# Performance work log

Hardware: AMD Instinct MI355X
Metric: run time of the kernel (lower is better)

Reference implementation:

```python
import jax, jax.numpy as jnp
import numpy as np

N, E = 50000, 600000
IN, PE, H, L, K = 112, 16, 128, 64, 4


def setup_inputs() -> dict:
    key = jax.random.key(0)
    ks = jax.random.split(key, 8)
    x = jax.random.normal(ks[0], (N, IN), jnp.float32)
    edge_index = jax.random.randint(ks[1], (2, E), 0, N, dtype=jnp.int64)
    lap_pe = jax.random.normal(ks[2], (N, PE), jnp.float32)
    edge_weight = jax.random.uniform(ks[3], (E,), jnp.float32)
    s = lambda k, shp, fan: jax.random.normal(k, shp, jnp.float32) / np.sqrt(fan).astype(np.float32)
    W1 = s(ks[4], (K, IN + PE, H), IN + PE)
    b1 = jnp.zeros((H,), jnp.float32)
    W2 = s(ks[5], (K, H, H), H)
    b2 = jnp.zeros((H,), jnp.float32)
    Wmu = s(ks[6], (H, L), H)
    bmu = jnp.zeros((L,), jnp.float32)
    Wlv = s(ks[7], (H, L), H)
    blv = jnp.zeros((L,), jnp.float32)
    return dict(x=x, edge_index=edge_index, lap_pe=lap_pe, edge_weight=edge_weight,
                W1=W1, b1=b1, W2=W2, b2=b2, Wmu=Wmu, bmu=bmu, Wlv=Wlv, blv=blv)


def _cheb_conv(h, src, dst, w, W, b):
    """PyG ChebConv with precomputed scaled-Laplacian edge weights w.
    T_0 = h ; T_1 = That h ; T_k = 2 That T_{k-1} - T_{k-2}; out = sum_k T_k W_k + b."""
    n = h.shape[0]
    prop = lambda t: jax.ops.segment_sum(w[:, None] * t[src], dst, num_segments=n)
    Tx0 = h
    out = Tx0 @ W[0]
    Tx1 = prop(Tx0)
    out = out + Tx1 @ W[1]
    for k in range(2, W.shape[0]):
        Tx2 = 2.0 * prop(Tx1) - Tx0
        out = out + Tx2 @ W[k]
        Tx0, Tx1 = Tx1, Tx2
    return out + b


def reference(x, edge_index, lap_pe, edge_weight, W1, b1, W2, b2, Wmu, bmu, Wlv, blv):
    n = x.shape[0]
    src, dst = edge_index[0], edge_index[1]
    # sym-normalized Laplacian, lambda_max=2 -> That = L_sym - I = -D^-1/2 A D^-1/2
    deg = jax.ops.segment_sum(edge_weight, src, num_segments=n)
    dis = jnp.where(deg > 0, jax.lax.rsqrt(jnp.maximum(deg, 1e-12)), 0.0)
    w = -dis[src] * edge_weight * dis[dst]
    h = jnp.concatenate([x, lap_pe], axis=1)  # [N, in+pe]
    h = jax.nn.relu(_cheb_conv(h, src, dst, w, W1, b1))
    h = jax.nn.relu(_cheb_conv(h, src, dst, w, W2, b2))
    mu = h @ Wmu + bmu
    logvar = h @ Wlv + blv
    return (mu, logvar)
```

## Files before the change

kernel.cpp:

```cpp
#include <hip/hip_runtime.h>


typedef __bf16 bf16x8 __attribute__((ext_vector_type(8)));
typedef float f32x4 __attribute__((ext_vector_type(4)));
typedef unsigned int uint32;
typedef unsigned short ushort16;

__device__ inline ushort16 f2bf(float f) {
    uint32 x = __float_as_uint(f);
    uint32 r = x + 0x7fffu + ((x >> 16) & 1u);
    return (ushort16)(r >> 16);
}
__device__ inline float bflo(uint32 v) { return __uint_as_float(v << 16); }
__device__ inline float bfhi(uint32 v) { return __uint_as_float(v & 0xffff0000u); }


__global__ void k_deg_cnt(const int* __restrict__ src, const int* __restrict__ dst,
                          const float* __restrict__ ew, float* __restrict__ deg,
                          int* __restrict__ cnt, int E) {
    int e = blockIdx.x * blockDim.x + threadIdx.x;
    if (e >= E) return;
    atomicAdd(&deg[src[e]], ew[e]);
    atomicAdd(&cnt[dst[e]], 1);
}

__global__ void k_dis(const float* __restrict__ deg, float* __restrict__ dis, int N) {
    int i = blockIdx.x * blockDim.x + threadIdx.x;
    if (i >= N) return;
    float d = deg[i];
    dis[i] = d > 0.f ? rsqrtf(fmaxf(d, 1e-12f)) : 0.f;
}

__global__ void k_scan_blk(const int* __restrict__ cnt, int* __restrict__ row_ptr,
                           int* __restrict__ blk_sums, int N) {
    __shared__ int wsum[4];
    const int tid = threadIdx.x;
    const int base = blockIdx.x * 1024 + tid * 4;
    int4 v = make_int4(0, 0, 0, 0);
    if (base + 3 < N) v = *(const int4*)&cnt[base];
    else {
        if (base + 0 < N) v.x = cnt[base + 0];
        if (base + 1 < N) v.y = cnt[base + 1];
        if (base + 2 < N) v.z = cnt[base + 2];
    }
    const int tsum = v.x + v.y + v.z + v.w;
    const int lane = tid & 63;
    const int wv = tid >> 6;
    int incl = tsum;
    #pragma unroll
    for (int off = 1; off < 64; off <<= 1) {
        int t = __shfl_up(incl, off);
        if (lane >= off) incl += t;
    }
    if (lane == 63) wsum[wv] = incl;
    __syncthreads();
    int woff = 0;
    #pragma unroll
    for (int w = 0; w < 4; ++w) if (w < wv) woff += wsum[w];
    const int excl = woff + incl - tsum;
    if (base + 0 < N) row_ptr[base + 0] = excl;
    if (base + 1 < N) row_ptr[base + 1] = excl + v.x;
    if (base + 2 < N) row_ptr[base + 2] = excl + v.x + v.y;
    if (base + 3 < N) row_ptr[base + 3] = excl + v.x + v.y + v.z;
    if (tid == 255) blk_sums[blockIdx.x] = woff + incl;
}

__global__ void k_scan_top(int* __restrict__ blk_sums, int* __restrict__ row_ptr,
                           int nblk, int N) {
    const int lane = threadIdx.x;
    int v = (lane < nblk) ? blk_sums[lane] : 0;
    int incl = v;
    #pragma unroll
    for (int off = 1; off < 64; off <<= 1) {
        int t = __shfl_up(incl, off);
        if (lane >= off) incl += t;
    }
    if (lane < nblk) blk_sums[lane] = incl - v;
    if (lane == 63) row_ptr[N] = incl;
}

__global__ void k_scan_fix(int* __restrict__ row_ptr, int* __restrict__ cursor,
                           const int* __restrict__ blk_sums, int N) {
    int i = blockIdx.x * blockDim.x + threadIdx.x;
    if (i >= N) return;
    int v = row_ptr[i] + blk_sums[i >> 10];
    row_ptr[i] = v;
    cursor[i] = v;
}

__global__ void k_scatter(const int* __restrict__ src, const int* __restrict__ dst,
                          const float* __restrict__ ew, const float* __restrict__ dis,
                          int* __restrict__ cursor, int* __restrict__ csr_src,
                          float* __restrict__ csr_w, int E) {
    int e = blockIdx.x * blockDim.x + threadIdx.x;
    if (e >= E) return;
    int s = src[e], d = dst[e];
    float wv = -dis[s] * ew[e] * dis[d];
    int pos = atomicAdd(&cursor[d], 1);
    csr_src[pos] = s;
    csr_w[pos] = wv;
}


__global__ void k_concat_bf16(const float* __restrict__ x, const float* __restrict__ pe,
                              uint32* __restrict__ h, int N) {
    int i = blockIdx.x * blockDim.x + threadIdx.x;
    if (i >= N * 64) return;
    int node = i >> 6, p = i & 63;
    float f0, f1;
    if (p < 56) { f0 = x[node * 112 + p * 2]; f1 = x[node * 112 + p * 2 + 1]; }
    else { int q = (p - 56) * 2; f0 = pe[node * 16 + q]; f1 = pe[node * 16 + q + 1]; }
    h[i] = (uint32)f2bf(f0) | ((uint32)f2bf(f1) << 16);
}


__global__ void k_pack_w(const float* __restrict__ W, ushort16* __restrict__ Wp, int KS) {
    int t = blockIdx.x * blockDim.x + threadIdx.x;
    if (t >= KS * 8 * 64) return;
    int l = t & 63, c = (t >> 6) & 7, ks = t >> 9;
    int k0 = ks * 32 + (l >> 4) * 8;
    int col = c * 16 + (l & 15);
    uint4 o;
    uint32 v[8];
    #pragma unroll
    for (int j = 0; j < 8; ++j) v[j] = f2bf(W[(size_t)(k0 + j) * 128 + col]);
    o.x = v[0] | (v[1] << 16); o.y = v[2] | (v[3] << 16);
    o.z = v[4] | (v[5] << 16); o.w = v[6] | (v[7] << 16);
    *(uint4*)(Wp + (size_t)t * 8) = o;
}

__global__ void k_pack_head(const float* __restrict__ Wm, const float* __restrict__ Wl,
                            ushort16* __restrict__ Wp) {
    int t = blockIdx.x * blockDim.x + threadIdx.x;
    if (t >= 4 * 8 * 64) return;
    int l = t & 63, c = (t >> 6) & 7, ks = t >> 9;
    int k0 = ks * 32 + (l >> 4) * 8;
    int cc = c * 16 + (l & 15);
    const float* Ws = (cc < 64) ? Wm : Wl;
    int col = cc & 63;
    uint4 o;
    uint32 v[8];
    #pragma unroll
    for (int j = 0; j < 8; ++j) v[j] = f2bf(Ws[(size_t)(k0 + j) * 64 + col]);
    o.x = v[0] | (v[1] << 16); o.y = v[2] | (v[3] << 16);
    o.z = v[4] | (v[5] << 16); o.w = v[6] | (v[7] << 16);
    *(uint4*)(Wp + (size_t)t * 8) = o;
}


template<bool HAS_SUB>
__global__ void k_prop_bf16(const ushort16* __restrict__ tin, const ushort16* __restrict__ sub,
                            float scale, const int* __restrict__ row_ptr,
                            const int* __restrict__ csr_src, const float* __restrict__ csr_w,
                            uint32* __restrict__ out, int N) {
    int wid = (blockIdx.x * blockDim.x + threadIdx.x) >> 6;
    int lane = threadIdx.x & 63;
    if (wid >= N) return;
    int beg = row_ptr[wid], end = row_ptr[wid + 1];
    float ax = 0.f, ay = 0.f;
    for (int base = beg; base < end; base += 64) {
        int m = end - base; if (m > 64) m = 64;
        int si = 0; float wv = 0.f;
        if (lane < m) { si = csr_src[base + lane]; wv = csr_w[base + lane]; }
        int j = 0;
        for (; j + 3 < m; j += 4) {
            int s0 = __shfl(si, j),     s1 = __shfl(si, j + 1);
            int s2 = __shfl(si, j + 2), s3 = __shfl(si, j + 3);
            float w0 = __shfl(wv, j),     w1 = __shfl(wv, j + 1);
            float w2 = __shfl(wv, j + 2), w3 = __shfl(wv, j + 3);
            uint32 v0 = *(const uint32*)((const ushort16*)tin + (size_t)s0 * 128 + lane * 2);
            uint32 v1 = *(const uint32*)((const ushort16*)tin + (size_t)s1 * 128 + lane * 2);
            uint32 v2 = *(const uint32*)((const ushort16*)tin + (size_t)s2 * 128 + lane * 2);
            uint32 v3 = *(const uint32*)((const ushort16*)tin + (size_t)s3 * 128 + lane * 2);
            ax = fmaf(w0, bflo(v0), ax); ay = fmaf(w0, bfhi(v0), ay);
            ax = fmaf(w1, bflo(v1), ax); ay = fmaf(w1, bfhi(v1), ay);
            ax = fmaf(w2, bflo(v2), ax); ay = fmaf(w2, bfhi(v2), ay);
            ax = fmaf(w3, bflo(v3), ax); ay = fmaf(w3, bfhi(v3), ay);
        }
        for (; j < m; ++j) {
            int s0 = __shfl(si, j);
            float w0 = __shfl(wv, j);
            uint32 v0 = *(const uint32*)((const ushort16*)tin + (size_t)s0 * 128 + lane * 2);
            ax = fmaf(w0, bflo(v0), ax); ay = fmaf(w0, bfhi(v0), ay);
        }
    }
    float ox = scale * ax, oy = scale * ay;
    if (HAS_SUB) {
        uint32 sv = *(const uint32*)((const ushort16*)sub + (size_t)wid * 128 + lane * 2);
        ox -= bflo(sv); oy -= bfhi(sv);
    }
    out[(size_t)wid * 64 + lane] = (uint32)f2bf(ox) | ((uint32)f2bf(oy) << 16);
}


template<bool RELU>
__launch_bounds__(256)
__global__ void k_mfma_gemm512(const ushort16* __restrict__ t0, const ushort16* __restrict__ t1,
                               const ushort16* __restrict__ t2, const ushort16* __restrict__ t3,
                               const ushort16* __restrict__ Wp, const float* __restrict__ bias,
                               ushort16* __restrict__ C, int N) {
    const int lane = threadIdx.x & 63;
    const int wave = threadIdx.x >> 6;
    const int brow = blockIdx.x * 128 + wave * 32;
    int r0 = brow + (lane & 15);
    int r1 = r0 + 16;
    if (r0 >= N) r0 = N - 1;
    if (r1 >= N) r1 = N - 1;
    const int kg8 = (lane >> 4) * 8;
    f32x4 acc[2][8] = {};
    #pragma unroll
    for (int t = 0; t < 4; ++t) {
        const ushort16* __restrict__ A = (t == 0) ? t0 : (t == 1) ? t1 : (t == 2) ? t2 : t3;
        const ushort16* a0p = A + (size_t)r0 * 128 + kg8;
        const ushort16* a1p = A + (size_t)r1 * 128 + kg8;
        #pragma unroll
        for (int ks2 = 0; ks2 < 4; ++ks2) {
            bf16x8 a0 = *(const bf16x8*)(a0p + ks2 * 32);
            bf16x8 a1 = *(const bf16x8*)(a1p + ks2 * 32);
            const ushort16* bp = Wp + (size_t)((t * 4 + ks2) * 8 * 64 + lane) * 8;
            #pragma unroll
            for (int c = 0; c < 8; ++c) {
                bf16x8 b = *(const bf16x8*)(bp + c * 512);
                acc[0][c] = __builtin_amdgcn_mfma_f32_16x16x32_bf16(a0, b, acc[0][c], 0, 0, 0);
                acc[1][c] = __builtin_amdgcn_mfma_f32_16x16x32_bf16(a1, b, acc[1][c], 0, 0, 0);
            }
        }
    }
    const int col0 = lane & 15;
    const int rj = (lane >> 4) * 4;
    #pragma unroll
    for (int m = 0; m < 2; ++m) {
        #pragma unroll
        for (int c = 0; c < 8; ++c) {
            float bv = bias[c * 16 + col0];
            #pragma unroll
            for (int j = 0; j < 4; ++j) {
                int row = brow + m * 16 + rj + j;
                if (row < N) {
                    float v = acc[m][c][j] + bv;
                    if (RELU) v = fmaxf(v, 0.f);
                    C[(size_t)row * 128 + c * 16 + col0] = f2bf(v);
                }
            }
        }
    }
}


__launch_bounds__(256)
__global__ void k_mfma_head(const ushort16* __restrict__ A, const ushort16* __restrict__ Wp,
                            const float* __restrict__ bm, const float* __restrict__ bl,
                            float* __restrict__ out, int N) {
    const int lane = threadIdx.x & 63;
    const int wave = threadIdx.x >> 6;
    const int brow = blockIdx.x * 128 + wave * 32;
    int r0 = brow + (lane & 15);
    int r1 = r0 + 16;
    if (r0 >= N) r0 = N - 1;
    if (r1 >= N) r1 = N - 1;
    const int kg8 = (lane >> 4) * 8;
    f32x4 acc[2][8] = {};
    const ushort16* a0p = A + (size_t)r0 * 128 + kg8;
    const ushort16* a1p = A + (size_t)r1 * 128 + kg8;
    #pragma unroll
    for (int ks = 0; ks < 4; ++ks) {
        bf16x8 a0 = *(const bf16x8*)(a0p + ks * 32);
        bf16x8 a1 = *(const bf16x8*)(a1p + ks * 32);
        const ushort16* bp = Wp + (size_t)(ks * 8 * 64 + lane) * 8;
        #pragma unroll
        for (int c = 0; c < 8; ++c) {
            bf16x8 b = *(const bf16x8*)(bp + c * 512);
            acc[0][c] = __builtin_amdgcn_mfma_f32_16x16x32_bf16(a0, b, acc[0][c], 0, 0, 0);
            acc[1][c] = __builtin_amdgcn_mfma_f32_16x16x32_bf16(a1, b, acc[1][c], 0, 0, 0);
        }
    }
    const int col0 = lane & 15;
    const int rj = (lane >> 4) * 4;
    #pragma unroll
    for (int m = 0; m < 2; ++m) {
        #pragma unroll
        for (int c = 0; c < 8; ++c) {
            int gcol = (c & 3) * 16 + col0;
            float bv = (c < 4) ? bm[gcol] : bl[gcol];
            size_t hoff = (c < 4) ? 0 : (size_t)N * 64;
            #pragma unroll
            for (int j = 0; j < 4; ++j) {
                int row = brow + m * 16 + rj + j;
                if (row < N)
                    out[hoff + (size_t)row * 64 + gcol] = acc[m][c][j] + bv;
            }
        }
    }
}


extern "C" void kernel_launch(void* const* d_in, const int* in_sizes, int n_in,
                              void* d_out, int out_size, void* d_ws, size_t ws_size,
                              hipStream_t stream) {
    const float* x   = (const float*)d_in[0];
    const int*   ei  = (const int*)d_in[1];
    const float* pe  = (const float*)d_in[2];
    const float* ew  = (const float*)d_in[3];
    const float* W1  = (const float*)d_in[4];
    const float* b1  = (const float*)d_in[5];
    const float* W2  = (const float*)d_in[6];
    const float* b2  = (const float*)d_in[7];
    const float* Wmu = (const float*)d_in[8];
    const float* bmu = (const float*)d_in[9];
    const float* Wlv = (const float*)d_in[10];
    const float* blv = (const float*)d_in[11];

    const int N = in_sizes[0] / 112;
    const int E = in_sizes[1] / 2;
    const int* src = ei;
    const int* dst = ei + E;

    char* ws = (char*)d_ws;
    size_t off = 0;
    auto alloc = [&](size_t bytes) -> char* {
        char* p = ws + off;
        off = (off + bytes + 255) & ~(size_t)255;
        return p;
    };
    float* deg     = (float*)alloc((size_t)N * 4);
    int*   cnt     = (int*)  alloc((size_t)N * 4);
    float* dis     = (float*)alloc((size_t)N * 4);
    int*   row_ptr = (int*)  alloc((size_t)(N + 1) * 4);
    int*   cursor  = (int*)  alloc((size_t)N * 4);
    int*   blk_sums= (int*)  alloc((size_t)256 * 4);
    int*   csr_src = (int*)  alloc((size_t)E * 4);
    float* csr_w   = (float*)alloc((size_t)E * 4);
    ushort16* W1p  = (ushort16*)alloc((size_t)512 * 128 * 2);
    ushort16* W2p  = (ushort16*)alloc((size_t)512 * 128 * 2);
    ushort16* WHp  = (ushort16*)alloc((size_t)128 * 128 * 2);
    ushort16* B0 = (ushort16*)alloc((size_t)N * 128 * 2);
    ushort16* B1 = (ushort16*)alloc((size_t)N * 128 * 2);
    ushort16* B2 = (ushort16*)alloc((size_t)N * 128 * 2);
    ushort16* B3 = (ushort16*)alloc((size_t)N * 128 * 2);
    ushort16* B4 = (ushort16*)alloc((size_t)N * 128 * 2);

    hipMemsetAsync(deg, 0, (size_t)N * 4, stream);
    hipMemsetAsync(cnt, 0, (size_t)N * 4, stream);

    const int eb = (E + 255) / 256;
    const int nb = (N + 255) / 256;
    const int pb = (N + 3) / 4;
    const int gb = (N + 127) / 128;
    const int nblk = (N + 1023) / 1024;

    k_deg_cnt<<<eb, 256, 0, stream>>>(src, dst, ew, deg, cnt, E);
    k_dis<<<nb, 256, 0, stream>>>(deg, dis, N);
    k_scan_blk<<<nblk, 256, 0, stream>>>(cnt, row_ptr, blk_sums, N);
    k_scan_top<<<1, 64, 0, stream>>>(blk_sums, row_ptr, nblk, N);
    k_scan_fix<<<nb, 256, 0, stream>>>(row_ptr, cursor, blk_sums, N);
    k_scatter<<<eb, 256, 0, stream>>>(src, dst, ew, dis, cursor, csr_src, csr_w, E);
    k_concat_bf16<<<(N * 64 + 255) / 256, 256, 0, stream>>>(x, pe, (uint32*)B0, N);
    k_pack_w<<<(16 * 8 * 64 + 255) / 256, 256, 0, stream>>>(W1, W1p, 16);
    k_pack_w<<<(16 * 8 * 64 + 255) / 256, 256, 0, stream>>>(W2, W2p, 16);
    k_pack_head<<<(4 * 8 * 64 + 255) / 256, 256, 0, stream>>>(Wmu, Wlv, WHp);

    k_prop_bf16<false><<<pb, 256, 0, stream>>>(B0, nullptr, 1.f, row_ptr, csr_src, csr_w, (uint32*)B1, N);
    k_prop_bf16<true ><<<pb, 256, 0, stream>>>(B1, B0, 2.f, row_ptr, csr_src, csr_w, (uint32*)B2, N);
    k_prop_bf16<true ><<<pb, 256, 0, stream>>>(B2, B1, 2.f, row_ptr, csr_src, csr_w, (uint32*)B3, N);
    k_mfma_gemm512<true><<<gb, 256, 0, stream>>>(B0, B1, B2, B3, W1p, b1, B4, N);

    k_prop_bf16<false><<<pb, 256, 0, stream>>>(B4, nullptr, 1.f, row_ptr, csr_src, csr_w, (uint32*)B0, N);
    k_prop_bf16<true ><<<pb, 256, 0, stream>>>(B0, B4, 2.f, row_ptr, csr_src, csr_w, (uint32*)B1, N);
    k_prop_bf16<true ><<<pb, 256, 0, stream>>>(B1, B0, 2.f, row_ptr, csr_src, csr_w, (uint32*)B2, N);
    k_mfma_gemm512<true><<<gb, 256, 0, stream>>>(B4, B0, B1, B2, W2p, b2, B3, N);

    k_mfma_head<<<gb, 256, 0, stream>>>(B3, WHp, bmu, blv, (float*)d_out, N);
}
```

Baseline: 357.0 us.

## Fold Chebyshev recurrence into weights and use plain powers of the propagation operator

Rewrites the Chebyshev basis as plain powers of That (T2=2P²-I, T3=4P³-3P) and folds the recombination into pre-transformed weight matrices. The propagation kernels then drop the scale and subtract steps. The CSR build stores src and weight interleaved as int2 and takes each slot from the count atomic, removing the cursor scan and the second atomic pass. Weight-packing and dis kernels are merged to cut launches. Dropping the recurrence changes rounding, since the bf16 intermediate powers are combined in the GEMM instead of step by step.

```diff
diff --git a/kernel.cpp b/kernel.cpp
--- a/kernel.cpp
+++ b/kernel.cpp
@@ -17,18 +17,11 @@
 
 __global__ void k_deg_cnt(const int* __restrict__ src, const int* __restrict__ dst,
                           const float* __restrict__ ew, float* __restrict__ deg,
-                          int* __restrict__ cnt, int E) {
+                          int* __restrict__ cnt, int* __restrict__ pos, int E) {
     int e = blockIdx.x * blockDim.x + threadIdx.x;
     if (e >= E) return;
     atomicAdd(&deg[src[e]], ew[e]);
-    atomicAdd(&cnt[dst[e]], 1);
-}
-
-__global__ void k_dis(const float* __restrict__ deg, float* __restrict__ dis, int N) {
-    int i = blockIdx.x * blockDim.x + threadIdx.x;
-    if (i >= N) return;
-    float d = deg[i];
-    dis[i] = d > 0.f ? rsqrtf(fmaxf(d, 1e-12f)) : 0.f;
+    pos[e] = atomicAdd(&cnt[dst[e]], 1);
 }
 
 __global__ void k_scan_blk(const int* __restrict__ cnt, int* __restrict__ row_ptr,
@@ -79,26 +72,24 @@
     if (lane == 63) row_ptr[N] = incl;
 }
 
-__global__ void k_scan_fix(int* __restrict__ row_ptr, int* __restrict__ cursor,
-                           const int* __restrict__ blk_sums, int N) {
+__global__ void k_fix_dis(int* __restrict__ row_ptr, const int* __restrict__ blk_sums,
+                          const float* __restrict__ deg, float* __restrict__ dis, int N) {
     int i = blockIdx.x * blockDim.x + threadIdx.x;
     if (i >= N) return;
-    int v = row_ptr[i] + blk_sums[i >> 10];
-    row_ptr[i] = v;
-    cursor[i] = v;
+    row_ptr[i] += blk_sums[i >> 10];
+    float d = deg[i];
+    dis[i] = d > 0.f ? rsqrtf(fmaxf(d, 1e-12f)) : 0.f;
 }
 
 __global__ void k_scatter(const int* __restrict__ src, const int* __restrict__ dst,
                           const float* __restrict__ ew, const float* __restrict__ dis,
-                          int* __restrict__ cursor, int* __restrict__ csr_src,
-                          float* __restrict__ csr_w, int E) {
+                          const int* __restrict__ row_ptr, const int* __restrict__ pos,
+                          int2* __restrict__ csr, int E) {
     int e = blockIdx.x * blockDim.x + threadIdx.x;
     if (e >= E) return;
     int s = src[e], d = dst[e];
     float wv = -dis[s] * ew[e] * dis[d];
-    int pos = atomicAdd(&cursor[d], 1);
-    csr_src[pos] = s;
-    csr_w[pos] = wv;
+    csr[row_ptr[d] + pos[e]] = make_int2(s, __float_as_int(wv));
 }
 
 
@@ -114,45 +105,55 @@
 }
 
 
-__global__ void k_pack_w(const float* __restrict__ W, ushort16* __restrict__ Wp, int KS) {
+__device__ inline float wtrans(const float* __restrict__ W, int kb, size_t o) {
+    switch (kb) {
+        case 0:  return W[o] - W[o + 32768];
+        case 1:  return W[o + 16384] - 3.f * W[o + 49152];
+        case 2:  return 2.f * W[o + 32768];
+        default: return 4.f * W[o + 49152];
+    }
+}
+
+__global__ void k_pack_all(const float* __restrict__ W1, const float* __restrict__ W2,
+                           const float* __restrict__ Wm, const float* __restrict__ Wl,
+                           ushort16* __restrict__ W1p, ushort16* __restrict__ W2p,
+                           ushort16* __restrict__ WHp) {
     int t = blockIdx.x * blockDim.x + threadIdx.x;
-    if (t >= KS * 8 * 64) return;
-    int l = t & 63, c = (t >> 6) & 7, ks = t >> 9;
-    int k0 = ks * 32 + (l >> 4) * 8;
-    int col = c * 16 + (l & 15);
-    uint4 o;
     uint32 v[8];
-    #pragma unroll
-    for (int j = 0; j < 8; ++j) v[j] = f2bf(W[(size_t)(k0 + j) * 128 + col]);
-    o.x = v[0] | (v[1] << 16); o.y = v[2] | (v[3] << 16);
-    o.z = v[4] | (v[5] << 16); o.w = v[6] | (v[7] << 16);
-    *(uint4*)(Wp + (size_t)t * 8) = o;
-}
-
-__global__ void k_pack_head(const float* __restrict__ Wm, const float* __restrict__ Wl,
-                            ushort16* __restrict__ Wp) {
-    int t = blockIdx.x * blockDim.x + threadIdx.x;
-    if (t >= 4 * 8 * 64) return;
-    int l = t & 63, c = (t >> 6) & 7, ks = t >> 9;
-    int k0 = ks * 32 + (l >> 4) * 8;
-    int cc = c * 16 + (l & 15);
-    const float* Ws = (cc < 64) ? Wm : Wl;
-    int col = cc & 63;
-    uint4 o;
-    uint32 v[8];
-    #pragma unroll
-    for (int j = 0; j < 8; ++j) v[j] = f2bf(Ws[(size_t)(k0 + j) * 64 + col]);
-    o.x = v[0] | (v[1] << 16); o.y = v[2] | (v[3] << 16);
-    o.z = v[4] | (v[5] << 16); o.w = v[6] | (v[7] << 16);
-    *(uint4*)(Wp + (size_t)t * 8) = o;
-}
-
-
-template<bool HAS_SUB>
-__global__ void k_prop_bf16(const ushort16* __restrict__ tin, const ushort16* __restrict__ sub,
-                            float scale, const int* __restrict__ row_ptr,
-                            const int* __restrict__ csr_src, const float* __restrict__ csr_w,
-                            uint32* __restrict__ out, int N) {
+    if (t < 16384) {
+        const float* W = (t < 8192) ? W1 : W2;
+        ushort16* Wp = (t < 8192) ? W1p : W2p;
+        int tt = t & 8191;
+        int l = tt & 63, c = (tt >> 6) & 7, ks = tt >> 9;
+        int kb = ks >> 2;
+        int r0 = (ks & 3) * 32 + (l >> 4) * 8;
+        int col = c * 16 + (l & 15);
+        #pragma unroll
+        for (int j = 0; j < 8; ++j)
+            v[j] = f2bf(wtrans(W, kb, (size_t)(r0 + j) * 128 + col));
+        uint4 o;
+        o.x = v[0] | (v[1] << 16); o.y = v[2] | (v[3] << 16);
+        o.z = v[4] | (v[5] << 16); o.w = v[6] | (v[7] << 16);
+        *(uint4*)(Wp + (size_t)tt * 8) = o;
+    } else if (t < 16384 + 2048) {
+        int tt = t - 16384;
+        int l = tt & 63, c = (tt >> 6) & 7, ks = tt >> 9;
+        int k0 = ks * 32 + (l >> 4) * 8;
+        int cc = c * 16 + (l & 15);
+        const float* Ws = (cc < 64) ? Wm : Wl;
+        int col = cc & 63;
+        #pragma unroll
+        for (int j = 0; j < 8; ++j) v[j] = f2bf(Ws[(size_t)(k0 + j) * 64 + col]);
+        uint4 o;
+        o.x = v[0] | (v[1] << 16); o.y = v[2] | (v[3] << 16);
+        o.z = v[4] | (v[5] << 16); o.w = v[6] | (v[7] << 16);
+        *(uint4*)(WHp + (size_t)tt * 8) = o;
+    }
+}
+
+
+__global__ void k_prop(const uint32* __restrict__ tin, const int2* __restrict__ csr,
+                       const int* __restrict__ row_ptr, uint32* __restrict__ out, int N) {
     int wid = (blockIdx.x * blockDim.x + threadIdx.x) >> 6;
     int lane = threadIdx.x & 63;
     if (wid >= N) return;
@@ -160,36 +161,18 @@
     float ax = 0.f, ay = 0.f;
     for (int base = beg; base < end; base += 64) {
         int m = end - base; if (m > 64) m = 64;
-        int si = 0; float wv = 0.f;
-        if (lane < m) { si = csr_src[base + lane]; wv = csr_w[base + lane]; }
-        int j = 0;
-        for (; j + 3 < m; j += 4) {
-            int s0 = __shfl(si, j),     s1 = __shfl(si, j + 1);
-            int s2 = __shfl(si, j + 2), s3 = __shfl(si, j + 3);
-            float w0 = __shfl(wv, j),     w1 = __shfl(wv, j + 1);
-            float w2 = __shfl(wv, j + 2), w3 = __shfl(wv, j + 3);
-            uint32 v0 = *(const uint32*)((const ushort16*)tin + (size_t)s0 * 128 + lane * 2);
-            uint32 v1 = *(const uint32*)((const ushort16*)tin + (size_t)s1 * 128 + lane * 2);
-            uint32 v2 = *(const uint32*)((const ushort16*)tin + (size_t)s2 * 128 + lane * 2);
-            uint32 v3 = *(const uint32*)((const ushort16*)tin + (size_t)s3 * 128 + lane * 2);
-            ax = fmaf(w0, bflo(v0), ax); ay = fmaf(w0, bfhi(v0), ay);
-            ax = fmaf(w1, bflo(v1), ax); ay = fmaf(w1, bfhi(v1), ay);
-            ax = fmaf(w2, bflo(v2), ax); ay = fmaf(w2, bfhi(v2), ay);
-            ax = fmaf(w3, bflo(v3), ax); ay = fmaf(w3, bfhi(v3), ay);
-        }
-        for (; j < m; ++j) {
-            int s0 = __shfl(si, j);
-            float w0 = __shfl(wv, j);
-            uint32 v0 = *(const uint32*)((const ushort16*)tin + (size_t)s0 * 128 + lane * 2);
-            ax = fmaf(w0, bflo(v0), ax); ay = fmaf(w0, bfhi(v0), ay);
-        }
-    }
-    float ox = scale * ax, oy = scale * ay;
-    if (HAS_SUB) {
-        uint32 sv = *(const uint32*)((const ushort16*)sub + (size_t)wid * 128 + lane * 2);
-        ox -= bflo(sv); oy -= bfhi(sv);
-    }
-    out[(size_t)wid * 64 + lane] = (uint32)f2bf(ox) | ((uint32)f2bf(oy) << 16);
+        int2 ev = (lane < m) ? csr[base + lane] : make_int2(0, 0);
+        for (int j = 0; j < m; j += 8) {
+            #pragma unroll
+            for (int u = 0; u < 8; ++u) {
+                int s = __shfl(ev.x, j + u);
+                float w = __uint_as_float(__shfl(ev.y, j + u));
+                uint32 v = tin[(size_t)s * 64 + lane];
+                ax = fmaf(w, bflo(v), ax); ay = fmaf(w, bfhi(v), ay);
+            }
+        }
+    }
+    out[(size_t)wid * 64 + lane] = (uint32)f2bf(ax) | ((uint32)f2bf(ay) << 16);
 }
 
 
@@ -326,10 +309,9 @@
     int*   cnt     = (int*)  alloc((size_t)N * 4);
     float* dis     = (float*)alloc((size_t)N * 4);
     int*   row_ptr = (int*)  alloc((size_t)(N + 1) * 4);
-    int*   cursor  = (int*)  alloc((size_t)N * 4);
     int*   blk_sums= (int*)  alloc((size_t)256 * 4);
-    int*   csr_src = (int*)  alloc((size_t)E * 4);
-    float* csr_w   = (float*)alloc((size_t)E * 4);
+    int*   pos     = (int*)  alloc((size_t)E * 4);
+    int2*  csr     = (int2*) alloc((size_t)E * 8);
     ushort16* W1p  = (ushort16*)alloc((size_t)512 * 128 * 2);
     ushort16* W2p  = (ushort16*)alloc((size_t)512 * 128 * 2);
     ushort16* WHp  = (ushort16*)alloc((size_t)128 * 128 * 2);
@@ -348,25 +330,22 @@
     const int gb = (N + 127) / 128;
     const int nblk = (N + 1023) / 1024;
 
-    k_deg_cnt<<<eb, 256, 0, stream>>>(src, dst, ew, deg, cnt, E);
-    k_dis<<<nb, 256, 0, stream>>>(deg, dis, N);
+    k_deg_cnt<<<eb, 256, 0, stream>>>(src, dst, ew, deg, cnt, pos, E);
     k_scan_blk<<<nblk, 256, 0, stream>>>(cnt, row_ptr, blk_sums, N);
     k_scan_top<<<1, 64, 0, stream>>>(blk_sums, row_ptr, nblk, N);
-    k_scan_fix<<<nb, 256, 0, stream>>>(row_ptr, cursor, blk_sums, N);
-    k_scatter<<<eb, 256, 0, stream>>>(src, dst, ew, dis, cursor, csr_src, csr_w, E);
+    k_fix_dis<<<nb, 256, 0, stream>>>(row_ptr, blk_sums, deg, dis, N);
+    k_scatter<<<eb, 256, 0, stream>>>(src, dst, ew, dis, row_ptr, pos, csr, E);
     k_concat_bf16<<<(N * 64 + 255) / 256, 256, 0, stream>>>(x, pe, (uint32*)B0, N);
-    k_pack_w<<<(16 * 8 * 64 + 255) / 256, 256, 0, stream>>>(W1, W1p, 16);
-    k_pack_w<<<(16 * 8 * 64 + 255) / 256, 256, 0, stream>>>(W2, W2p, 16);
-    k_pack_head<<<(4 * 8 * 64 + 255) / 256, 256, 0, stream>>>(Wmu, Wlv, WHp);
-
-    k_prop_bf16<false><<<pb, 256, 0, stream>>>(B0, nullptr, 1.f, row_ptr, csr_src, csr_w, (uint32*)B1, N);
-    k_prop_bf16<true ><<<pb, 256, 0, stream>>>(B1, B0, 2.f, row_ptr, csr_src, csr_w, (uint32*)B2, N);
-    k_prop_bf16<true ><<<pb, 256, 0, stream>>>(B2, B1, 2.f, row_ptr, csr_src, csr_w, (uint32*)B3, N);
+    k_pack_all<<<(16384 + 2048 + 255) / 256, 256, 0, stream>>>(W1, W2, Wmu, Wlv, W1p, W2p, WHp);
+
+    k_prop<<<pb, 256, 0, stream>>>((uint32*)B0, csr, row_ptr, (uint32*)B1, N);
+    k_prop<<<pb, 256, 0, stream>>>((uint32*)B1, csr, row_ptr, (uint32*)B2, N);
+    k_prop<<<pb, 256, 0, stream>>>((uint32*)B2, csr, row_ptr, (uint32*)B3, N);
     k_mfma_gemm512<true><<<gb, 256, 0, stream>>>(B0, B1, B2, B3, W1p, b1, B4, N);
 
-    k_prop_bf16<false><<<pb, 256, 0, stream>>>(B4, nullptr, 1.f, row_ptr, csr_src, csr_w, (uint32*)B0, N);
-    k_prop_bf16<true ><<<pb, 256, 0, stream>>>(B0, B4, 2.f, row_ptr, csr_src, csr_w, (uint32*)B1, N);
-    k_prop_bf16<true ><<<pb, 256, 0, stream>>>(B1, B0, 2.f, row_ptr, csr_src, csr_w, (uint32*)B2, N);
+    k_prop<<<pb, 256, 0, stream>>>((uint32*)B4, csr, row_ptr, (uint32*)B0, N);
+    k_prop<<<pb, 256, 0, stream>>>((uint32*)B0, csr, row_ptr, (uint32*)B1, N);
+    k_prop<<<pb, 256, 0, stream>>>((uint32*)B1, csr, row_ptr, (uint32*)B2, N);
     k_mfma_gemm512<true><<<gb, 256, 0, stream>>>(B4, B0, B1, B2, W2p, b2, B3, N);
 
     k_mfma_head<<<gb, 256, 0, stream>>>(B3, WHp, bmu, blv, (float*)d_out, N);
```

Result: faster. 306.2 us (-14.2%).
